# Performance work log

Hardware: AMD Instinct MI355X
Metric: run time of the kernel (lower is better)

## Reference

```python
import jax, jax.numpy as jnp
import numpy as np

N_NODES = 50000
N_EDGES = 800000
INPUT_DIM = 8
HIDDEN_DIM = 128


def setup_inputs() -> dict:
    key = jax.random.key(0)
    k = jax.random.split(key, 8)
    x = jax.random.normal(k[0], (N_NODES, INPUT_DIM), dtype=jnp.float32)
    edge_index = jax.random.randint(k[1], (2, N_EDGES), 0, N_NODES, dtype=jnp.int64)
    edge_attr = jax.random.uniform(k[2], (N_EDGES, 1), dtype=jnp.float32)
    node_embedding = jax.random.normal(k[3], (N_NODES, HIDDEN_DIM), dtype=jnp.float32)
    # Linear weights stored as [in, out] so y = x @ W (bias=False everywhere)
    s1 = 1.0 / np.sqrt(INPUT_DIM)
    sh = 1.0 / np.sqrt(HIDDEN_DIM)
    W1 = jax.random.uniform(k[4], (INPUT_DIM, HIDDEN_DIM), jnp.float32, -s1, s1)
    W2 = jax.random.uniform(k[5], (HIDDEN_DIM, HIDDEN_DIM), jnp.float32, -sh, sh)
    W3 = jax.random.uniform(k[6], (HIDDEN_DIM, HIDDEN_DIM), jnp.float32, -sh, sh)
    W4 = jax.random.uniform(k[7], (1, HIDDEN_DIM), jnp.float32, -1.0, 1.0)
    return {"x": x, "edge_index": edge_index, "edge_attr": edge_attr,
            "node_embedding": node_embedding, "W1": W1, "W2": W2, "W3": W3, "W4": W4}


def reference(x, edge_index, edge_attr, node_embedding, W1, W2, W3, W4):
    n = x.shape[0]
    row, col = edge_index[0], edge_index[1]
    # theta_1(x): [N, hidden]
    node_feature_embedding = x @ W1
    # gather neighbor embeddings along edges, scatter-sum to destination rows
    node_embedding_aggr = jax.ops.segment_sum(node_embedding[col], row, num_segments=n)
    # relu(theta_4(edge_attr)): [E, hidden], then scatter-sum to rows
    edge_feature_embedding = jax.nn.relu(edge_attr @ W4)
    edge_embedding_aggr = jax.ops.segment_sum(edge_feature_embedding, row, num_segments=n)
    return jax.nn.relu(node_feature_embedding + node_embedding_aggr @ W2 + edge_embedding_aggr @ W3)
```

## Files before the change

kernel.cpp:

```cpp
#include <hip/hip_runtime.h>

#define N_NODES 50000
#define N_EDGES 800000
#define IN_DIM  8
#define HD      128
#define N_SCAN_BLOCKS ((N_NODES + 255) / 256)
#define NREP 16
#define NTILES ((N_NODES + 63) / 64)
#define N_HIST_BLOCKS (N_EDGES / 256)
#define NRANGE 8
#define RANGE_N (N_NODES / NRANGE)
#define N_HISTB (NREP * NRANGE)
#define GRID_P1 (N_HISTB + NTILES)
#define GRID_PREP 2

typedef unsigned short ushort_t;
typedef unsigned int uint_t;
typedef __attribute__((ext_vector_type(8))) short short8;
typedef __attribute__((ext_vector_type(4))) float float4v;
typedef __attribute__((ext_vector_type(4))) int int4v;
typedef __attribute__((ext_vector_type(2))) uint_t uint2v;

static __device__ inline unsigned short f2bf(float f) {
    unsigned u = __float_as_uint(f);
    unsigned r = (u + 0x7FFF + ((u >> 16) & 1)) >> 16;
    return (unsigned short)r;
}
static __device__ inline float bf2f(unsigned short b) {
    return __uint_as_float(((unsigned)b) << 16);
}

__global__ void prep_kernel(const float* __restrict__ W2,
                            short8* __restrict__ blob,
                            const float* __restrict__ W4,
                            const float* __restrict__ W3,
                            float* __restrict__ v3,
                            int* __restrict__ bsums) {
    int t = threadIdx.x;
    if (blockIdx.x == 0) {
#pragma unroll
        for (int i = 0; i < 8; ++i) {
            int slot = t * 8 + i;
            int f    = slot >> 6;
            int lane = slot & 63;
            int ct = f >> 2, ki = f & 3;
            int n16 = lane & 15, quad = lane >> 4;
            short8 fr;
#pragma unroll
            for (int j = 0; j < 8; ++j) {
                int k = ki * 32 + quad * 8 + j;
                fr[j] = (short)f2bf(W2[k * HD + ct * 16 + n16]);
            }
            blob[slot] = fr;
        }
        return;
    }
    bsums[t] = 0;
    if (t < HD) {
        float acc = 0.f;
        for (int k = 0; k < HD; ++k) {
            float w = W4[k];
            w = w > 0.f ? w : 0.f;
            acc += w * W3[k * HD + t];
        }
        v3[t] = acc;
    }
}

__global__ __launch_bounds__(256, 2)
void phase1_kernel(const float* __restrict__ emb,
                   const short8* __restrict__ blob,
                   ushort_t* __restrict__ T16,
                   const int* __restrict__ ei,
                   int* __restrict__ cnt,
                   ushort_t* __restrict__ rank16) {
    __shared__ uint_t hcnt[RANGE_N];
    int t = threadIdx.x;

    if (blockIdx.x < N_HISTB) {
        int rep   = blockIdx.x & (NREP - 1);
        int range = blockIdx.x / NREP;
        int rbase = range * RANGE_N;
        for (int i = t; i < RANGE_N; i += 256) hcnt[i] = 0u;
        __syncthreads();
        int g    = t >> 6;
        int lane = t & 63;
        int NC = (N_HIST_BLOCKS - rep + NREP - 1) / NREP;
        for (int j0 = 0; j0 < NC; j0 += 4) {
            int j = j0 + g;
            if (j < NC) {
                int c  = rep + j * NREP;
                int e0 = c * 256 + lane * 4;
                int4v rv = *(const int4v*)(ei + e0);
#pragma unroll
                for (int q = 0; q < 4; ++q) {
                    int lr = rv[q] - rbase;
                    if ((unsigned)lr < (unsigned)RANGE_N) {
                        uint_t rk = atomicAdd(&hcnt[lr], 1u);
                        rank16[e0 + q] = (ushort_t)rk;
                    }
                }
            }
        }
        __syncthreads();
        int* crow = cnt + rep * N_NODES + rbase;
        for (int i = t; i < RANGE_N; i += 256) crow[i] = (int)hcnt[i];
        return;
    }

    int tt   = blockIdx.x - N_HISTB;
    int wave = t >> 6;
    int lane = t & 63;
    int n16  = lane & 15;
    int quad = lane >> 4;

    short8 wfrag[8][4];
#pragma unroll
    for (int ct = 0; ct < 8; ++ct)
#pragma unroll
        for (int ki = 0; ki < 4; ++ki)
            wfrag[ct][ki] = blob[(ct * 4 + ki) * 64 + lane];

    int rowbase = tt * 64 + wave * 16;
    int row  = rowbase + n16;
    int rowc = row < N_NODES ? row : N_NODES - 1;
    const float4v* arow = (const float4v*)(emb + (size_t)rowc * HD);

    short8 efrag[4];
#pragma unroll
    for (int ki = 0; ki < 4; ++ki) {
        float4v lo = __builtin_nontemporal_load(&arow[ki * 8 + quad * 2]);
        float4v hi = __builtin_nontemporal_load(&arow[ki * 8 + quad * 2 + 1]);
        short8 a;
        a[0] = (short)f2bf(lo[0]); a[1] = (short)f2bf(lo[1]);
        a[2] = (short)f2bf(lo[2]); a[3] = (short)f2bf(lo[3]);
        a[4] = (short)f2bf(hi[0]); a[5] = (short)f2bf(hi[1]);
        a[6] = (short)f2bf(hi[2]); a[7] = (short)f2bf(hi[3]);
        efrag[ki] = a;
    }

    float4v acc[8];
#pragma unroll
    for (int ct = 0; ct < 8; ++ct) acc[ct] = (float4v){0.f, 0.f, 0.f, 0.f};

#pragma unroll
    for (int ki = 0; ki < 4; ++ki)
#pragma unroll
        for (int ct = 0; ct < 8; ++ct)
            acc[ct] = __builtin_amdgcn_mfma_f32_16x16x32_bf16(
                wfrag[ct][ki], efrag[ki], acc[ct], 0, 0, 0);

    if (row < N_NODES) {
        ushort_t* dstu = T16 + (size_t)row * HD + quad * 4;
#pragma unroll
        for (int ct = 0; ct < 8; ++ct) {
            uint2v v;
            v[0] = (uint_t)f2bf(acc[ct][0]) | ((uint_t)f2bf(acc[ct][1]) << 16);
            v[1] = (uint_t)f2bf(acc[ct][2]) | ((uint_t)f2bf(acc[ct][3]) << 16);
            *(uint2v*)(dstu + ct * 16) = v;
        }
    }
}

__global__ void scan1_kernel(const int* __restrict__ cnt,
                             int* __restrict__ off,
                             int* __restrict__ bases,
                             int* __restrict__ bsums) {
    __shared__ int lds[256];
    int t = threadIdx.x;
    int n = blockIdx.x * 256 + t;
    int c[NREP];
    int tsum = 0;
#pragma unroll
    for (int r = 0; r < NREP; ++r) {
        c[r] = (n < N_NODES) ? cnt[r * N_NODES + n] : 0;
        tsum += c[r];
    }
    lds[t] = tsum;
    __syncthreads();
    for (int o = 1; o < 256; o <<= 1) {
        int add = (t >= o) ? lds[t - o] : 0;
        __syncthreads();
        lds[t] += add;
        __syncthreads();
    }
    int ex = lds[t] - tsum;
    int total = lds[255];
    if (n < N_NODES) {
        off[n] = ex;
        int run = ex;
#pragma unroll
        for (int r = 0; r < NREP; ++r) {
            bases[r * N_NODES + n] = run;
            run += c[r];
        }
    }
    for (int bb = blockIdx.x + 1 + t; bb < N_SCAN_BLOCKS; bb += 256)
        atomicAdd(&bsums[bb], total);
}

__global__ void fill_kernel(const int* __restrict__ ei,
                            const float* __restrict__ attr,
                            const ushort_t* __restrict__ rank16,
                            const int* __restrict__ bases,
                            const int* __restrict__ bsums,
                            uint_t* __restrict__ packed) {
    int e = blockIdx.x * 256 + threadIdx.x;
    int rep = (e >> 8) & (NREP - 1);
    int r = ei[e];
    int pos = bases[rep * N_NODES + r] + bsums[r >> 8] + (int)rank16[e];
    uint_t p = ((uint_t)f2bf(attr[e]) << 16) | (uint_t)ei[N_EDGES + e];
    packed[pos] = p;
}

__global__ void aggregate_kernel(const int* __restrict__ off,
                                 const int* __restrict__ bsums,
                                 const uint_t* __restrict__ packed,
                                 const ushort_t* __restrict__ T16,
                                 const float* __restrict__ x,
                                 const float* __restrict__ W1,
                                 const float* __restrict__ v3,
                                 float* __restrict__ out) {
    int tid  = blockIdx.x * 256 + threadIdx.x;
    int node = tid >> 4;
    int lane = tid & 15;
    int s  = off[node] + bsums[node >> 8];
    int e1 = (node + 1 == N_NODES) ? N_EDGES
                                   : off[node + 1] + bsums[(node + 1) >> 8];
    int deg = e1 - s;

    float acc[8];
#pragma unroll
    for (int i = 0; i < 8; ++i) acc[i] = 0.f;
    float ssum = 0.f;

    for (int base = 0; base < deg; base += 16) {
        int rem = deg - base; if (rem > 16) rem = 16;
        uint_t p = 0;
        if (lane < rem) p = __builtin_nontemporal_load(&packed[s + base + lane]);
        ssum += __uint_as_float(p & 0xFFFF0000u);
        int col = (int)(p & 0xFFFFu);
        int j = 0;
        for (; j + 4 <= rem; j += 4) {
            int c0 = __shfl(col, j + 0, 16);
            int c1 = __shfl(col, j + 1, 16);
            int c2 = __shfl(col, j + 2, 16);
            int c3 = __shfl(col, j + 3, 16);
            short8 t0 = ((const short8*)(T16 + (size_t)c0 * HD))[lane];
            short8 t1 = ((const short8*)(T16 + (size_t)c1 * HD))[lane];
            short8 t2 = ((const short8*)(T16 + (size_t)c2 * HD))[lane];
            short8 t3 = ((const short8*)(T16 + (size_t)c3 * HD))[lane];
#pragma unroll
            for (int i = 0; i < 8; ++i)
                acc[i] += (bf2f((ushort_t)t0[i]) + bf2f((ushort_t)t1[i]))
                        + (bf2f((ushort_t)t2[i]) + bf2f((ushort_t)t3[i]));
        }
        for (; j < rem; ++j) {
            int c = __shfl(col, j, 16);
            short8 tv = ((const short8*)(T16 + (size_t)c * HD))[lane];
#pragma unroll
            for (int i = 0; i < 8; ++i)
                acc[i] += bf2f((ushort_t)tv[i]);
        }
    }
    for (int o = 8; o; o >>= 1) ssum += __shfl_xor(ssum, o, 16);

    const float4v* v3p = (const float4v*)v3;
    float4v b0 = v3p[lane * 2], b1 = v3p[lane * 2 + 1];
    acc[0] += ssum * b0[0]; acc[1] += ssum * b0[1];
    acc[2] += ssum * b0[2]; acc[3] += ssum * b0[3];
    acc[4] += ssum * b1[0]; acc[5] += ssum * b1[1];
    acc[6] += ssum * b1[2]; acc[7] += ssum * b1[3];
#pragma unroll
    for (int i = 0; i < IN_DIM; ++i) {
        float xi = x[node * IN_DIM + i];
        const float4v* wp = (const float4v*)(W1 + i * HD);
        float4v w0 = wp[lane * 2], w1 = wp[lane * 2 + 1];
        acc[0] += xi * w0[0]; acc[1] += xi * w0[1];
        acc[2] += xi * w0[2]; acc[3] += xi * w0[3];
        acc[4] += xi * w1[0]; acc[5] += xi * w1[1];
        acc[6] += xi * w1[2]; acc[7] += xi * w1[3];
    }
    float4v o0, o1;
    o0[0] = fmaxf(acc[0], 0.f); o0[1] = fmaxf(acc[1], 0.f);
    o0[2] = fmaxf(acc[2], 0.f); o0[3] = fmaxf(acc[3], 0.f);
    o1[0] = fmaxf(acc[4], 0.f); o1[1] = fmaxf(acc[5], 0.f);
    o1[2] = fmaxf(acc[6], 0.f); o1[3] = fmaxf(acc[7], 0.f);
    float4v* op = (float4v*)(out + (size_t)node * HD);
    __builtin_nontemporal_store(o0, op + lane * 2);
    __builtin_nontemporal_store(o1, op + lane * 2 + 1);
}

extern "C" void kernel_launch(void* const* d_in, const int* in_sizes, int n_in,
                              void* d_out, int out_size, void* d_ws, size_t ws_size,
                              hipStream_t stream) {
    const float* x    = (const float*)d_in[0];
    const int*   ei   = (const int*)  d_in[1];
    const float* attr = (const float*)d_in[2];
    const float* emb  = (const float*)d_in[3];
    const float* W1   = (const float*)d_in[4];
    const float* W2   = (const float*)d_in[5];
    const float* W3   = (const float*)d_in[6];
    const float* W4   = (const float*)d_in[7];
    float* out = (float*)d_out;

    char* w = (char*)d_ws;
    uint_t*   packed = (uint_t*)w;
    ushort_t* T16    = (ushort_t*)(w + (size_t)N_EDGES * 4);
    short8*   blob   = (short8*)((char*)T16 + (size_t)N_NODES * HD * 2);
    int*      off    = (int*)((char*)blob + 2048 * 16);
    int*      bases  = off + N_NODES + 4;
    int*      cnt    = bases + NREP * N_NODES;
    int*      bsums  = cnt + NREP * N_NODES;
    float*    v3     = (float*)(bsums + 256);
    ushort_t* rank16 = (ushort_t*)(v3 + HD);

    prep_kernel  <<<GRID_PREP, 256, 0, stream>>>(W2, blob, W4, W3, v3, bsums);
    phase1_kernel<<<GRID_P1, 256, 0, stream>>>(emb, blob, T16, ei, cnt, rank16);
    scan1_kernel <<<N_SCAN_BLOCKS, 256, 0, stream>>>(cnt, off, bases, bsums);
    fill_kernel  <<<N_HIST_BLOCKS, 256, 0, stream>>>(ei, attr, rank16, bases, bsums, packed);
    aggregate_kernel<<<(N_NODES * 16) / 256, 256, 0, stream>>>(
        off, bsums, packed, T16, x, W1, v3, out);
}
```

Measured before the change: 180.1 us.

## Regroup kernels: merge prep into histogram, co-schedule scan with bf16 GEMM

The W2 blob prep and v3/bsums initialization now run as extra blocks of the histogram kernel, and the per-node GEMM producing T16 moves into a combined kernel alongside the prefix-scan blocks. This removes one kernel launch and lets the compute-heavy GEMM overlap the latency-bound scan instead of the histogram pass. The histogram loop also gains a software-prefetch of the next edge-index chunk. The cost is that the GEMM can no longer overlap the histogram pass, and its blocks share launch-bound register limits with the scan blocks.

```diff
diff --git a/kernel.cpp b/kernel.cpp
--- a/kernel.cpp
+++ b/kernel.cpp
@@ -11,8 +11,8 @@
 #define NRANGE 8
 #define RANGE_N (N_NODES / NRANGE)
 #define N_HISTB (NREP * NRANGE)
-#define GRID_P1 (N_HISTB + NTILES)
-#define GRID_PREP 2
+#define GRID_P1 (N_HISTB + 2)
+#define GRID_SG (N_SCAN_BLOCKS + NTILES)
 
 typedef unsigned short ushort_t;
 typedef unsigned int uint_t;
@@ -30,50 +30,17 @@
     return __uint_as_float(((unsigned)b) << 16);
 }
 
-__global__ void prep_kernel(const float* __restrict__ W2,
-                            short8* __restrict__ blob,
-                            const float* __restrict__ W4,
-                            const float* __restrict__ W3,
-                            float* __restrict__ v3,
-                            int* __restrict__ bsums) {
-    int t = threadIdx.x;
-    if (blockIdx.x == 0) {
-#pragma unroll
-        for (int i = 0; i < 8; ++i) {
-            int slot = t * 8 + i;
-            int f    = slot >> 6;
-            int lane = slot & 63;
-            int ct = f >> 2, ki = f & 3;
-            int n16 = lane & 15, quad = lane >> 4;
-            short8 fr;
-#pragma unroll
-            for (int j = 0; j < 8; ++j) {
-                int k = ki * 32 + quad * 8 + j;
-                fr[j] = (short)f2bf(W2[k * HD + ct * 16 + n16]);
-            }
-            blob[slot] = fr;
-        }
-        return;
-    }
-    bsums[t] = 0;
-    if (t < HD) {
-        float acc = 0.f;
-        for (int k = 0; k < HD; ++k) {
-            float w = W4[k];
-            w = w > 0.f ? w : 0.f;
-            acc += w * W3[k * HD + t];
-        }
-        v3[t] = acc;
-    }
-}
-
 __global__ __launch_bounds__(256, 2)
-void phase1_kernel(const float* __restrict__ emb,
-                   const short8* __restrict__ blob,
-                   ushort_t* __restrict__ T16,
+void phase1_kernel(const short8* ,
+                   const float* __restrict__ W2,
+                   short8* __restrict__ blob,
                    const int* __restrict__ ei,
                    int* __restrict__ cnt,
-                   ushort_t* __restrict__ rank16) {
+                   ushort_t* __restrict__ rank16,
+                   const float* __restrict__ W4,
+                   const float* __restrict__ W3,
+                   float* __restrict__ v3,
+                   int* __restrict__ bsums) {
     __shared__ uint_t hcnt[RANGE_N];
     int t = threadIdx.x;
 
@@ -86,21 +53,25 @@
         int g    = t >> 6;
         int lane = t & 63;
         int NC = (N_HIST_BLOCKS - rep + NREP - 1) / NREP;
-        for (int j0 = 0; j0 < NC; j0 += 4) {
-            int j = j0 + g;
-            if (j < NC) {
-                int c  = rep + j * NREP;
-                int e0 = c * 256 + lane * 4;
-                int4v rv = *(const int4v*)(ei + e0);
-#pragma unroll
-                for (int q = 0; q < 4; ++q) {
-                    int lr = rv[q] - rbase;
-                    if ((unsigned)lr < (unsigned)RANGE_N) {
-                        uint_t rk = atomicAdd(&hcnt[lr], 1u);
-                        rank16[e0 + q] = (ushort_t)rk;
-                    }
+        int j = g;
+        int4v rv = {0, 0, 0, 0};
+        if (j < NC)
+            rv = *(const int4v*)(ei + (rep + j * NREP) * 256 + lane * 4);
+        while (j < NC) {
+            int jn = j + 4;
+            int4v nx = {0, 0, 0, 0};
+            if (jn < NC)
+                nx = *(const int4v*)(ei + (rep + jn * NREP) * 256 + lane * 4);
+            int e0 = (rep + j * NREP) * 256 + lane * 4;
+#pragma unroll
+            for (int q = 0; q < 4; ++q) {
+                int lr = rv[q] - rbase;
+                if ((unsigned)lr < (unsigned)RANGE_N) {
+                    uint_t rk = atomicAdd(&hcnt[lr], 1u);
+                    rank16[e0 + q] = (ushort_t)rk;
                 }
             }
+            rv = nx; j = jn;
         }
         __syncthreads();
         int* crow = cnt + rep * N_NODES + rbase;
@@ -108,7 +79,82 @@
         return;
     }
 
-    int tt   = blockIdx.x - N_HISTB;
+    if (blockIdx.x == N_HISTB) {
+#pragma unroll
+        for (int i = 0; i < 8; ++i) {
+            int slot = t * 8 + i;
+            int f    = slot >> 6;
+            int lane = slot & 63;
+            int ct = f >> 2, ki = f & 3;
+            int n16 = lane & 15, quad = lane >> 4;
+            short8 fr;
+#pragma unroll
+            for (int jj = 0; jj < 8; ++jj) {
+                int k = ki * 32 + quad * 8 + jj;
+                fr[jj] = (short)f2bf(W2[k * HD + ct * 16 + n16]);
+            }
+            blob[slot] = fr;
+        }
+        return;
+    }
+
+    bsums[t] = 0;
+    if (t < HD) {
+        float acc = 0.f;
+        for (int k = 0; k < HD; ++k) {
+            float w = W4[k];
+            w = w > 0.f ? w : 0.f;
+            acc += w * W3[k * HD + t];
+        }
+        v3[t] = acc;
+    }
+}
+
+__global__ __launch_bounds__(256, 2)
+void scan_gemm_kernel(const int* __restrict__ cnt,
+                      int* __restrict__ off,
+                      int* __restrict__ bases,
+                      int* __restrict__ bsums,
+                      const float* __restrict__ emb,
+                      const short8* __restrict__ blob,
+                      ushort_t* __restrict__ T16) {
+    __shared__ int lds[256];
+    int t = threadIdx.x;
+
+    if (blockIdx.x < N_SCAN_BLOCKS) {
+        int n = blockIdx.x * 256 + t;
+        int c[NREP];
+        int tsum = 0;
+#pragma unroll
+        for (int r = 0; r < NREP; ++r) {
+            c[r] = (n < N_NODES) ? cnt[r * N_NODES + n] : 0;
+            tsum += c[r];
+        }
+        lds[t] = tsum;
+        __syncthreads();
+        for (int o = 1; o < 256; o <<= 1) {
+            int add = (t >= o) ? lds[t - o] : 0;
+            __syncthreads();
+            lds[t] += add;
+            __syncthreads();
+        }
+        int ex = lds[t] - tsum;
+        int total = lds[255];
+        if (n < N_NODES) {
+            off[n] = ex;
+            int run = ex;
+#pragma unroll
+            for (int r = 0; r < NREP; ++r) {
+                bases[r * N_NODES + n] = run;
+                run += c[r];
+            }
+        }
+        for (int bb = blockIdx.x + 1 + t; bb < N_SCAN_BLOCKS; bb += 256)
+            atomicAdd(&bsums[bb], total);
+        return;
+    }
+
+    int tt   = blockIdx.x - N_SCAN_BLOCKS;
     int wave = t >> 6;
     int lane = t & 63;
     int n16  = lane & 15;
@@ -160,43 +206,6 @@
             *(uint2v*)(dstu + ct * 16) = v;
         }
     }
-}
-
-__global__ void scan1_kernel(const int* __restrict__ cnt,
-                             int* __restrict__ off,
-                             int* __restrict__ bases,
-                             int* __restrict__ bsums) {
-    __shared__ int lds[256];
-    int t = threadIdx.x;
-    int n = blockIdx.x * 256 + t;
-    int c[NREP];
-    int tsum = 0;
-#pragma unroll
-    for (int r = 0; r < NREP; ++r) {
-        c[r] = (n < N_NODES) ? cnt[r * N_NODES + n] : 0;
-        tsum += c[r];
-    }
-    lds[t] = tsum;
-    __syncthreads();
-    for (int o = 1; o < 256; o <<= 1) {
-        int add = (t >= o) ? lds[t - o] : 0;
-        __syncthreads();
-        lds[t] += add;
-        __syncthreads();
-    }
-    int ex = lds[t] - tsum;
-    int total = lds[255];
-    if (n < N_NODES) {
-        off[n] = ex;
-        int run = ex;
-#pragma unroll
-        for (int r = 0; r < NREP; ++r) {
-            bases[r * N_NODES + n] = run;
-            run += c[r];
-        }
-    }
-    for (int bb = blockIdx.x + 1 + t; bb < N_SCAN_BLOCKS; bb += 256)
-        atomicAdd(&bsums[bb], total);
 }
 
 __global__ void fill_kernel(const int* __restrict__ ei,
@@ -315,9 +324,10 @@
     float*    v3     = (float*)(bsums + 256);
     ushort_t* rank16 = (ushort_t*)(v3 + HD);
 
-    prep_kernel  <<<GRID_PREP, 256, 0, stream>>>(W2, blob, W4, W3, v3, bsums);
-    phase1_kernel<<<GRID_P1, 256, 0, stream>>>(emb, blob, T16, ei, cnt, rank16);
-    scan1_kernel <<<N_SCAN_BLOCKS, 256, 0, stream>>>(cnt, off, bases, bsums);
+    phase1_kernel<<<GRID_P1, 256, 0, stream>>>(
+        (const short8*)blob, W2, blob, ei, cnt, rank16, W4, W3, v3, bsums);
+    scan_gemm_kernel<<<GRID_SG, 256, 0, stream>>>(
+        cnt, off, bases, bsums, emb, blob, T16);
     fill_kernel  <<<N_HIST_BLOCKS, 256, 0, stream>>>(ei, attr, rank16, bases, bsums, packed);
     aggregate_kernel<<<(N_NODES * 16) / 256, 256, 0, stream>>>(
         off, bsums, packed, T16, x, W1, v3, out);
```

New measurement: 188.5 us. 1.05x slower.
